# Kernel tuning notes

Measured on AMD Instinct MI355X. Metric: run time of the kernel, lower is better.

## Reference

```python
import jax, jax.numpy as jnp
import numpy as np

B, NSTEPS = 256, 128
I, H, V = 128, 1024, 1024  # input_size, hidden_size, output_size
SOS = 0


def setup_inputs() -> dict:
    key = jax.random.key(0)
    ks = jax.random.split(key, 9)
    s = 0.02
    return {
        "z": jax.random.normal(ks[0], (B, I), dtype=jnp.float32),
        "inputs": jax.random.randint(ks[1], (NSTEPS, B), 0, V, dtype=jnp.int64),
        "temperature": 10,  # randn() < 10 always -> teacher forcing every step
        "embed_w": jax.random.normal(ks[2], (V, H), dtype=jnp.float32) * s,
        "z2h_w": jax.random.normal(ks[3], (H, I), dtype=jnp.float32) * s,
        "z2h_b": jnp.zeros((H,), dtype=jnp.float32),
        "gru_w_ih": jax.random.normal(ks[4], (3 * H, H + I), dtype=jnp.float32) * s,
        "gru_b_ih": jnp.zeros((3 * H,), dtype=jnp.float32),
        "gru_w_hh": jax.random.normal(ks[5], (3 * H, H), dtype=jnp.float32) * s,
        "gru_b_hh": jnp.zeros((3 * H,), dtype=jnp.float32),
        "out_w": jax.random.normal(ks[6], (V, H + I), dtype=jnp.float32) * s,
        "out_b": jnp.zeros((V,), dtype=jnp.float32),
    }


def _gru_cell(x, h, w_ih, b_ih, w_hh, b_hh):
    # PyTorch GRU cell math
    gi = x @ w_ih.T + b_ih          # [B, 3H]
    gh = h @ w_hh.T + b_hh          # [B, 3H]
    i_r, i_z, i_n = jnp.split(gi, 3, axis=1)
    h_r, h_z, h_n = jnp.split(gh, 3, axis=1)
    r = jax.nn.sigmoid(i_r + h_r)
    zg = jax.nn.sigmoid(i_z + h_z)
    n = jnp.tanh(i_n + r * h_n)
    return (1.0 - zg) * n + zg * h


def reference(z, inputs, temperature, embed_w, z2h_w, z2h_b,
              gru_w_ih, gru_b_ih, gru_w_hh, gru_b_hh, out_w, out_b):
    # hidden init: z2h(z), n_layers=1 -> single [B, H] state
    h0 = z @ z2h_w.T + z2h_b
    tok0 = jnp.full((z.shape[0],), SOS, dtype=inputs.dtype)

    def step(carry, tok_next):
        tok, h = carry
        emb = jax.nn.relu(embed_w[tok])            # [B, H]
        x = jnp.concatenate([emb, z], axis=1)      # [B, H+I]
        h = _gru_cell(x, h, gru_w_ih, gru_b_ih, gru_w_hh, gru_b_hh)
        o = jnp.concatenate([h, z], axis=1) @ out_w.T + out_b  # [B, V]
        # teacher forcing (temperature >> randn always true): next input = inputs[i]
        return (tok_next, h), o

    (_, _), outs = jax.lax.scan(step, (tok0, h0), inputs)  # outs: [NSTEPS, B, V]
    return outs.transpose(1, 0, 2)  # [B, NSTEPS, V]
```

## Files before the change

### kernel.cpp

```cpp
#include <hip/hip_runtime.h>
#include <stdint.h>


#define NSTEP 128

typedef unsigned short u16;
typedef unsigned int u32;
typedef __attribute__((ext_vector_type(8))) short bf16x8;
typedef __attribute__((ext_vector_type(4))) int i32x4;
typedef __attribute__((ext_vector_type(4))) float f32x4;

typedef __attribute__((address_space(3))) void lds_void;
typedef const __attribute__((address_space(1))) void glb_void;
#define GLD16(g, l) __builtin_amdgcn_global_load_lds((glb_void*)(g), (lds_void*)(l), 16, 0, 0)
#define GLD16C(g, l) __builtin_amdgcn_global_load_lds((glb_void*)(g), (lds_void*)(l), 16, 0, 17)
#define CFENCE() asm volatile("" ::: "memory")
#define SCHEDB() __builtin_amdgcn_sched_barrier(0)

#if __has_builtin(__builtin_amdgcn_exp2f)
#define EXP2(x) __builtin_amdgcn_exp2f(x)
#else
#define EXP2(x) exp2f(x)
#endif
#if __has_builtin(__builtin_amdgcn_rcpf)
#define RCP(x) __builtin_amdgcn_rcpf(x)
#else
#define RCP(x) (1.0f / (x))
#endif

__device__ __forceinline__ u16 f2bf(float f) {
    u32 u = __float_as_uint(f);
    u = (u + 0x7FFFu + ((u >> 16) & 1u)) >> 16;
    return (u16)u;
}
__device__ __forceinline__ float fsigmoid(float x) {
    return RCP(1.f + EXP2(x * -1.44269504f));
}
__device__ __forceinline__ float ftanh(float x) {
    x = fminf(fmaxf(x, -18.f), 18.f);
    float t = EXP2(x * 2.88539008f);
    return (t - 1.f) * RCP(t + 1.f);
}

__device__ __forceinline__ void gloadf(float& d, const float* a) {
    asm volatile("global_load_dword %0, %1, off" : "=&v"(d) : "v"(a) : "memory");
}
__device__ __forceinline__ void gloadi4(i32x4& d, const int* a) {
    asm volatile("global_load_dwordx4 %0, %1, off" : "=&v"(d) : "v"(a) : "memory");
}
__device__ __forceinline__ void gstore_short_c(u16* a, u32 v) {
    asm volatile("global_store_short %0, %1, off sc0 sc1" ::"v"(a), "v"(v) : "memory");
}
__device__ __forceinline__ void gstoref(float* a, float v) {
    asm volatile("global_store_dword %0, %1, off" ::"v"(a), "v"(v) : "memory");
}

__global__ void cast_k(const float* __restrict__ src, int ld, int off, int relu,
                       u16* __restrict__ dst, int n) {
    for (int i = blockIdx.x * blockDim.x + threadIdx.x; i < n; i += gridDim.x * blockDim.x) {
        int row = i >> 10, col = i & 1023;
        float v = src[(long)row * ld + off + col];
        if (relu) v = fmaxf(v, 0.f);
        dst[i] = f2bf(v);
    }
}

__global__ void smallgemm_k(const float* __restrict__ z, const float* __restrict__ W,
                            int ldw, int off, const float* __restrict__ bias,
                            const float* __restrict__ bias2, int n2max,
                            float* __restrict__ C, u16* __restrict__ Cbf, int N) {
    int n = blockIdx.x;
    int b = threadIdx.x;
    float acc = bias[n] + ((bias2 && n < n2max) ? bias2[n] : 0.f);
    const float* zr = z + b * 128;
    const float* wr = W + (long)n * ldw + off;
#pragma unroll 8
    for (int k = 0; k < 128; ++k) acc += zr[k] * wr[k];
    C[b * N + n] = acc;
    if (Cbf) Cbf[b * N + n] = f2bf(acc);
}

__global__ __launch_bounds__(256) void egemm_k(const u16* __restrict__ A,
                                               const u16* __restrict__ W,
                                               float* __restrict__ C) {
    __shared__ __align__(16) u16 lds[2][160 * 64];
    int tid = threadIdx.x, lane = tid & 63, wv = tid >> 6;
    int r0 = (blockIdx.x & 31) * 32;
    int n0 = (blockIdx.x >> 5) * 128;

    f32x4 acc[2][2];
#pragma unroll
    for (int m = 0; m < 2; ++m)
#pragma unroll
        for (int n = 0; n < 2; ++n) acc[m][n] = (f32x4){0.f, 0.f, 0.f, 0.f};

    auto stage = [&](int k0, int bufi) {
#pragma unroll
        for (int r = 0; r < 5; ++r) {
            int L = r * 256 + tid;
            int row = L >> 3;
            int c4 = (L & 7) ^ (row & 7);
            const u16* src = (row < 32)
                                 ? A + (long)(r0 + row) * 1024 + k0 + c4 * 8
                                 : W + (long)(n0 + row - 32) * 1024 + k0 + c4 * 8;
            GLD16(src, &lds[bufi][L * 8]);
        }
    };
    stage(0, 0);
    stage(64, 1);
    for (int it = 0; it < 16; ++it) {
        if (it < 15) asm volatile("s_waitcnt vmcnt(5)" ::: "memory");
        else         asm volatile("s_waitcnt vmcnt(0)" ::: "memory");
        __builtin_amdgcn_s_barrier();
        const char* base = (const char*)&lds[it & 1][0];
        bf16x8 af[2][2], bfr[2][2];
#pragma unroll
        for (int ks = 0; ks < 2; ++ks)
#pragma unroll
            for (int q = 0; q < 2; ++q) {
                int kb = ks * 64 + ((lane >> 4) << 4);
                int rowa = q * 16 + (lane & 15);
                af[ks][q] = *(const bf16x8*)(base + rowa * 128 + (kb ^ ((rowa & 7) << 4)));
                int rowb = 32 + wv * 32 + q * 16 + (lane & 15);
                bfr[ks][q] = *(const bf16x8*)(base + rowb * 128 + (kb ^ ((rowb & 7) << 4)));
            }
#pragma unroll
        for (int ks = 0; ks < 2; ++ks)
#pragma unroll
            for (int m = 0; m < 2; ++m)
#pragma unroll
                for (int n = 0; n < 2; ++n)
                    acc[m][n] = __builtin_amdgcn_mfma_f32_16x16x32_bf16(af[ks][m], bfr[ks][n],
                                                                        acc[m][n], 0, 0, 0);
        asm volatile("s_waitcnt lgkmcnt(0)" ::: "memory");
        __builtin_amdgcn_s_barrier();
        if (it + 2 < 16) stage((it + 2) * 64, it & 1);
    }
#pragma unroll
    for (int m = 0; m < 2; ++m)
#pragma unroll
        for (int n = 0; n < 2; ++n)
#pragma unroll
            for (int r = 0; r < 4; ++r) {
                int row = r0 + m * 16 + ((lane >> 4) << 2) + r;
                int col = n0 + wv * 32 + n * 16 + (lane & 15);
                C[(long)row * 3072 + col] = acc[m][n][r];
            }
}

__global__ __launch_bounds__(256, 1) void decoder_k(
    const u16* __restrict__ Whh,
    const u16* __restrict__ Wout,
    const float* __restrict__ E,
    const float* __restrict__ Zih2,
    const float* __restrict__ Zout,
    const float* __restrict__ bhh,
    const int* __restrict__ toks,
    const float* __restrict__ h0f,
    u16* __restrict__ Hx,
    float* __restrict__ out,
    u32* __restrict__ flags) {
    __shared__ __align__(16) char L[163840];
    const int tid = threadIdx.x, lane = tid & 63, wv = tid >> 6;
    const int bid = blockIdx.x;
    const int rB = bid >> 6;
    const int c = bid & 63;

#pragma unroll
    for (int r = 0; r < 8; ++r) {
        int l = r * 256 + tid, row = l >> 7, ck = (l & 127) ^ (row & 15);
        GLD16(Whh + (long)(c * 16 + row) * 1024 + ck * 8, &L[65536 + l * 16]);
    }
#pragma unroll
    for (int r = 0; r < 8; ++r) {
        int l = r * 256 + tid, row = l >> 7, ck = (l & 127) ^ (row & 15);
        GLD16(Whh + (long)(1024 + c * 16 + row) * 1024 + ck * 8, &L[98304 + l * 16]);
    }
    asm volatile("s_waitcnt vmcnt(0)" ::: "memory");
    __builtin_amdgcn_s_barrier();
    bf16x8 w0[32], w1[32];
#pragma unroll
    for (int it = 0; it < 8; ++it)
#pragma unroll
        for (int ks = 0; ks < 4; ++ks) {
            int row = lane & 15, kc = it * 16 + ks * 4 + (lane >> 4);
            w0[it * 4 + ks] = *(const bf16x8*)(L + 65536 + row * 2048 + ((kc ^ row) << 4));
            w1[it * 4 + ks] = *(const bf16x8*)(L + 98304 + row * 2048 + ((kc ^ row) << 4));
        }
    asm volatile("s_waitcnt lgkmcnt(0)" ::: "memory");
    __builtin_amdgcn_s_barrier();
#pragma unroll
    for (int r = 0; r < 8; ++r) {
        int l = r * 256 + tid, row = l >> 7, ck = (l & 127) ^ (row & 15);
        GLD16(Whh + (long)(2048 + c * 16 + row) * 1024 + ck * 8, &L[l * 16]);
    }
#pragma unroll
    for (int r = 0; r < 8; ++r) {
        int l = r * 256 + tid, row = l >> 7, ck = (l & 127) ^ (row & 15);
        GLD16(Wout + (long)(c * 16 + row) * 1024 + ck * 8, &L[32768 + l * 16]);
    }
    asm volatile("s_waitcnt vmcnt(0)" ::: "memory");
    __builtin_amdgcn_s_barrier();

    const int bbase = rB * 64 + wv * 16 + ((lane >> 4) << 2);
    const int j = c * 16 + (lane & 15);
    const float bhn = bhh[2048 + j];
    float hprev[4], zi0[4], zi1[4], zi2[4], zo[4];
#pragma unroll
    for (int r = 0; r < 4; ++r) {
        int b = bbase + r;
        hprev[r] = h0f[b * 1024 + j];
        zi0[r] = Zih2[(long)b * 3072 + j];
        zi1[r] = Zih2[(long)b * 3072 + 1024 + j];
        zi2[r] = Zih2[(long)b * 3072 + 2048 + j];
        zo[r] = Zout[b * 1024 + j];
    }

    float ec0[4], ec1[4], ec2[4], en0[4], en1[4], en2[4];
#pragma unroll
    for (int r = 0; r < 4; ++r) {
        const float* eb = E + j;
        gloadf(en0[r], eb);
        gloadf(en1[r], eb + 1024);
        gloadf(en2[r], eb + 2048);
    }

    for (int s = 0; s <= NSTEP; ++s) {
        i32x4 tokv;
        if (s < NSTEP) gloadi4(tokv, toks + s * 256 + bbase);

        const u16* hsrc = Hx + (size_t)(s & 1) * 262144;
        auto stage = [&](int ch) {
            char* dst = L + 65536 + (ch % 6) * 16384;
            int k0 = ch * 128;
#pragma unroll
            for (int r = 0; r < 4; ++r) {
                int l = r * 256 + tid, row = l >> 4, ck = (l & 15) ^ (row & 15);
                GLD16C(hsrc + (long)(rB * 64 + row) * 1024 + k0 + ck * 8, dst + l * 16);
            }
        };
        stage(0);
        stage(1);
        stage(2);
        stage(3);
        CFENCE();

        if (s >= 1) {
            if (tid < 64) {
                const u32 tgt = (u32)s;
                const u32* gf = flags + (rB << 6) + 32;
                while (true) {
                    u32 v = __hip_atomic_load(gf + (lane & 31), __ATOMIC_RELAXED,
                                              __HIP_MEMORY_SCOPE_AGENT);
                    if (__all(v >= tgt)) break;
                    __builtin_amdgcn_s_sleep(1);
                }
            }
            __builtin_amdgcn_s_barrier();
        }

        f32x4 a0 = {0.f, 0.f, 0.f, 0.f}, a1 = a0, a2 = a0, aO = a0;
#pragma unroll
        for (int it = 0; it < 8; ++it) {
            if (it < 4) stage(it + 4);
            if (it < 4)       asm volatile("s_waitcnt vmcnt(16)" ::: "memory");
            else if (it == 4) asm volatile("s_waitcnt vmcnt(12)" ::: "memory");
            else if (it == 5) asm volatile("s_waitcnt vmcnt(8)" ::: "memory");
            else if (it == 6) asm volatile("s_waitcnt vmcnt(4)" ::: "memory");
            else              asm volatile("s_waitcnt vmcnt(0)" ::: "memory");
            SCHEDB();
            __builtin_amdgcn_s_barrier();
            const char* Ab = L + 65536 + (it % 6) * 16384;
            bf16x8 af[4];
#pragma unroll
            for (int ks = 0; ks < 4; ++ks) {
                int row = wv * 16 + (lane & 15), kc = ks * 4 + (lane >> 4);
                af[ks] = *(const bf16x8*)(Ab + row * 256 + ((kc ^ (row & 15)) << 4));
            }
#pragma unroll
            for (int ks = 0; ks < 4; ++ks)
                a0 = __builtin_amdgcn_mfma_f32_16x16x32_bf16(af[ks], w0[it * 4 + ks], a0, 0, 0, 0);
#pragma unroll
            for (int ks = 0; ks < 4; ++ks)
                a1 = __builtin_amdgcn_mfma_f32_16x16x32_bf16(af[ks], w1[it * 4 + ks], a1, 0, 0, 0);
#pragma unroll
            for (int ks = 0; ks < 4; ++ks) {
                int row = lane & 15, kc = it * 16 + ks * 4 + (lane >> 4);
                bf16x8 wg = *(const bf16x8*)(L + row * 2048 + ((kc ^ row) << 4));
                a2 = __builtin_amdgcn_mfma_f32_16x16x32_bf16(af[ks], wg, a2, 0, 0, 0);
            }
#pragma unroll
            for (int ks = 0; ks < 4; ++ks) {
                int row = lane & 15, kc = it * 16 + ks * 4 + (lane >> 4);
                bf16x8 wo = *(const bf16x8*)(L + 32768 + row * 2048 + ((kc ^ row) << 4));
                aO = __builtin_amdgcn_mfma_f32_16x16x32_bf16(af[ks], wo, aO, 0, 0, 0);
            }
        }
        if (s < NSTEP) {
#pragma unroll
            for (int r = 0; r < 4; ++r) {
                ec0[r] = en0[r];
                ec1[r] = en1[r];
                ec2[r] = en2[r];
            }
        }

        if (s < NSTEP) {
            u16* hdst = Hx + (size_t)((s + 1) & 1) * 262144;
#pragma unroll
            for (int r = 0; r < 4; ++r) {
                float rg = fsigmoid(ec0[r] + zi0[r] + a0[r]);
                float zg = fsigmoid(ec1[r] + zi1[r] + a1[r]);
                float nn = ftanh(ec2[r] + zi2[r] + rg * (a2[r] + bhn));
                float hv = (1.f - zg) * nn + zg * hprev[r];
                hprev[r] = hv;
                gstore_short_c(hdst + (bbase + r) * 1024 + j, (u32)f2bf(hv));
            }
        }
        if (s >= 1) {
#pragma unroll
            for (int r = 0; r < 4; ++r)
                gstoref(out + (long)(bbase + r) * 131072 + (long)(s - 1) * 1024 + j,
                        aO[r] + zo[r]);
        }
        if (s < NSTEP) {
#pragma unroll
            for (int r = 0; r < 4; ++r) {
                const float* eb = E + (long)tokv[r] * 3072 + j;
                gloadf(en0[r], eb);
                gloadf(en1[r], eb + 1024);
                gloadf(en2[r], eb + 2048);
            }
            if (s >= 1) asm volatile("s_waitcnt vmcnt(16)" ::: "memory");
            else        asm volatile("s_waitcnt vmcnt(12)" ::: "memory");
            SCHEDB();
            __builtin_amdgcn_s_barrier();
            if (tid == 0)
                __hip_atomic_store(&flags[bid], (u32)(s + 1), __ATOMIC_RELAXED,
                                   __HIP_MEMORY_SCOPE_AGENT);
            if (tid < 64) {
                const u32 tgt = (u32)(s + 1);
                const u32* gf = flags + (rB << 6);
                while (true) {
                    u32 v = __hip_atomic_load(gf + (lane & 31), __ATOMIC_RELAXED,
                                              __HIP_MEMORY_SCOPE_AGENT);
                    if (__all(v >= tgt)) break;
                    __builtin_amdgcn_s_sleep(1);
                }
            }
            __builtin_amdgcn_s_barrier();
        }
    }
}

extern "C" void kernel_launch(void* const* d_in, const int* in_sizes, int n_in,
                              void* d_out, int out_size, void* d_ws, size_t ws_size,
                              hipStream_t stream) {
    const float* z = (const float*)d_in[0];
    const int* toks = (const int*)d_in[1];
    const float* embed_w = (const float*)d_in[3];
    const float* z2h_w = (const float*)d_in[4];
    const float* z2h_b = (const float*)d_in[5];
    const float* w_ih = (const float*)d_in[6];
    const float* b_ih = (const float*)d_in[7];
    const float* w_hh = (const float*)d_in[8];
    const float* b_hh = (const float*)d_in[9];
    const float* out_w = (const float*)d_in[10];
    const float* out_b = (const float*)d_in[11];
    float* out = (float*)d_out;

    char* ws = (char*)d_ws;
    size_t off = 0;
    auto alloc = [&](size_t bytes) {
        char* p = ws + off;
        off += (bytes + 255) & ~(size_t)255;
        return p;
    };
    u16* Whh_bf = (u16*)alloc(3072ull * 1024 * 2);
    u16* Wout_bf = (u16*)alloc(1024ull * 1024 * 2);
    u16* Wihh_bf = (u16*)alloc(3072ull * 1024 * 2);
    u16* Emb_bf = (u16*)alloc(1024ull * 1024 * 2);
    float* E = (float*)alloc(1024ull * 3072 * 4);
    float* Zih = (float*)alloc(256ull * 3072 * 4);
    float* Zout = (float*)alloc(256ull * 1024 * 4);
    float* hf = (float*)alloc(256ull * 1024 * 4);
    u16* Hx = (u16*)alloc(2ull * 256 * 1024 * 2);
    u32* flags = (u32*)alloc(1024);

    hipMemsetAsync(flags, 0, 1024, stream);
    cast_k<<<2048, 256, 0, stream>>>(w_hh, 1024, 0, 0, Whh_bf, 3072 * 1024);
    cast_k<<<2048, 256, 0, stream>>>(out_w, 1152, 0, 0, Wout_bf, 1024 * 1024);
    cast_k<<<2048, 256, 0, stream>>>(w_ih, 1152, 0, 0, Wihh_bf, 3072 * 1024);
    cast_k<<<1024, 256, 0, stream>>>(embed_w, 1024, 0, 1, Emb_bf, 1024 * 1024);
    smallgemm_k<<<1024, 256, 0, stream>>>(z, z2h_w, 128, 0, z2h_b, nullptr, 0, hf, Hx, 1024);
    smallgemm_k<<<3072, 256, 0, stream>>>(z, w_ih, 1152, 1024, b_ih, b_hh, 2048, Zih, nullptr, 3072);
    smallgemm_k<<<1024, 256, 0, stream>>>(z, out_w, 1152, 1024, out_b, nullptr, 0, Zout, nullptr, 1024);
    egemm_k<<<768, 256, 0, stream>>>(Emb_bf, Wihh_bf, E);

    decoder_k<<<256, 256, 0, stream>>>(Whh_bf, Wout_bf, E, Zih, Zout, b_hh, toks, hf, Hx, out,
                                       flags);
}
```

Baseline: 1.117 ms.

## Split decoder into 512 XCC-local blocks with register-resident output weights

```diff
diff --git a/kernel.cpp b/kernel.cpp
--- a/kernel.cpp
+++ b/kernel.cpp
@@ -14,6 +14,7 @@
 typedef const __attribute__((address_space(1))) void glb_void;
 #define GLD16(g, l) __builtin_amdgcn_global_load_lds((glb_void*)(g), (lds_void*)(l), 16, 0, 0)
 #define GLD16C(g, l) __builtin_amdgcn_global_load_lds((glb_void*)(g), (lds_void*)(l), 16, 0, 17)
+#define GLD16S0(g, l) __builtin_amdgcn_global_load_lds((glb_void*)(g), (lds_void*)(l), 16, 0, 1)
 #define CFENCE() asm volatile("" ::: "memory")
 #define SCHEDB() __builtin_amdgcn_sched_barrier(0)
 
@@ -51,8 +52,29 @@
 __device__ __forceinline__ void gstore_short_c(u16* a, u32 v) {
     asm volatile("global_store_short %0, %1, off sc0 sc1" ::"v"(a), "v"(v) : "memory");
 }
+__device__ __forceinline__ void gstore_short_p(u16* a, u32 v) {
+    asm volatile("global_store_short %0, %1, off" ::"v"(a), "v"(v) : "memory");
+}
 __device__ __forceinline__ void gstoref(float* a, float v) {
     asm volatile("global_store_dword %0, %1, off" ::"v"(a), "v"(v) : "memory");
+}
+__device__ __forceinline__ void gstoreu32_c(u32* a, u32 v) {
+    asm volatile("global_store_dword %0, %1, off sc0 sc1" ::"v"(a), "v"(v) : "memory");
+}
+__device__ __forceinline__ void gstoreu32_p(u32* a, u32 v) {
+    asm volatile("global_store_dword %0, %1, off" ::"v"(a), "v"(v) : "memory");
+}
+__device__ __forceinline__ u32 pollload_s0(const u32* a) {
+    u32 d;
+    asm volatile("global_load_dword %0, %1, off sc0\n\ts_waitcnt vmcnt(0)"
+                 : "=&v"(d) : "v"(a) : "memory");
+    return d;
+}
+__device__ __forceinline__ u32 pollload_c(const u32* a) {
+    u32 d;
+    asm volatile("global_load_dword %0, %1, off sc0 sc1\n\ts_waitcnt vmcnt(0)"
+                 : "=&v"(d) : "v"(a) : "memory");
+    return d;
 }
 
 __global__ void cast_k(const float* __restrict__ src, int ld, int off, int relu,
@@ -148,7 +170,7 @@
             }
 }
 
-__global__ __launch_bounds__(256, 1) void decoder_k(
+__global__ __launch_bounds__(128, 1) void decoder_k(
     const u16* __restrict__ Whh,
     const u16* __restrict__ Wout,
     const float* __restrict__ E,
@@ -159,50 +181,68 @@
     const float* __restrict__ h0f,
     u16* __restrict__ Hx,
     float* __restrict__ out,
-    u32* __restrict__ flags) {
-    __shared__ __align__(16) char L[163840];
+    u32* __restrict__ flags,
+    u32* __restrict__ xcctab) {
+    __shared__ __align__(16) char L[81920];
     const int tid = threadIdx.x, lane = tid & 63, wv = tid >> 6;
     const int bid = blockIdx.x;
-    const int rB = bid >> 6;
-    const int c = bid & 63;
-
-#pragma unroll
-    for (int r = 0; r < 8; ++r) {
-        int l = r * 256 + tid, row = l >> 7, ck = (l & 127) ^ (row & 15);
-        GLD16(Whh + (long)(c * 16 + row) * 1024 + ck * 8, &L[65536 + l * 16]);
-    }
-#pragma unroll
-    for (int r = 0; r < 8; ++r) {
-        int l = r * 256 + tid, row = l >> 7, ck = (l & 127) ^ (row & 15);
-        GLD16(Whh + (long)(1024 + c * 16 + row) * 1024 + ck * 8, &L[98304 + l * 16]);
-    }
+    const int g = bid & 7;
+    const int c = bid >> 3;
+
+    u32 myxcc;
+    asm volatile("s_getreg_b32 %0, hwreg(HW_REG_XCC_ID)" : "=s"(myxcc));
+    if (tid == 0) gstoreu32_c(xcctab + bid, myxcc);
     asm volatile("s_waitcnt vmcnt(0)" ::: "memory");
     __builtin_amdgcn_s_barrier();
-    bf16x8 w0[32], w1[32];
-#pragma unroll
-    for (int it = 0; it < 8; ++it)
-#pragma unroll
-        for (int ks = 0; ks < 4; ++ks) {
-            int row = lane & 15, kc = it * 16 + ks * 4 + (lane >> 4);
-            w0[it * 4 + ks] = *(const bf16x8*)(L + 65536 + row * 2048 + ((kc ^ row) << 4));
-            w1[it * 4 + ks] = *(const bf16x8*)(L + 98304 + row * 2048 + ((kc ^ row) << 4));
-        }
-    asm volatile("s_waitcnt lgkmcnt(0)" ::: "memory");
+    int lok;
+    if (tid < 64) {
+        u32 xv;
+        while (true) {
+            xv = pollload_c(xcctab + (g << 6) + lane);
+            SCHEDB();
+            if (__all(xv != 0xFFFFFFFFu)) break;
+            __builtin_amdgcn_s_sleep(1);
+        }
+        u32 x0 = __builtin_amdgcn_readfirstlane(xv);
+        int ok = __all(xv == x0) ? 1 : 0;
+        if (tid == 0) *(volatile int*)&L[0] = ok;
+    }
     __builtin_amdgcn_s_barrier();
-#pragma unroll
-    for (int r = 0; r < 8; ++r) {
-        int l = r * 256 + tid, row = l >> 7, ck = (l & 127) ^ (row & 15);
+    lok = *(volatile int*)&L[0];
+    __builtin_amdgcn_s_barrier();
+
+    bf16x8 w0[32], w1[32], wO[32];
+    auto wload = [&](const u16* base, int rowoff, bf16x8* wreg) {
+#pragma unroll
+        for (int r = 0; r < 16; ++r) {
+            int l = r * 128 + tid, row = l >> 7, ck = (l & 127) ^ (row & 15);
+            GLD16(base + (long)(rowoff + c * 16 + row) * 1024 + ck * 8, &L[32768 + l * 16]);
+        }
+        asm volatile("s_waitcnt vmcnt(0)" ::: "memory");
+        __builtin_amdgcn_s_barrier();
+#pragma unroll
+        for (int it = 0; it < 8; ++it)
+#pragma unroll
+            for (int ks = 0; ks < 4; ++ks) {
+                int row = lane & 15, kc = it * 16 + ks * 4 + (lane >> 4);
+                wreg[it * 4 + ks] =
+                    *(const bf16x8*)(L + 32768 + row * 2048 + ((kc ^ row) << 4));
+            }
+        asm volatile("s_waitcnt lgkmcnt(0)" ::: "memory");
+        __builtin_amdgcn_s_barrier();
+    };
+    wload(Whh, 0, w0);
+    wload(Whh, 1024, w1);
+    wload(Wout, 0, wO);
+#pragma unroll
+    for (int r = 0; r < 16; ++r) {
+        int l = r * 128 + tid, row = l >> 7, ck = (l & 127) ^ (row & 15);
         GLD16(Whh + (long)(2048 + c * 16 + row) * 1024 + ck * 8, &L[l * 16]);
-    }
-#pragma unroll
-    for (int r = 0; r < 8; ++r) {
-        int l = r * 256 + tid, row = l >> 7, ck = (l & 127) ^ (row & 15);
-        GLD16(Wout + (long)(c * 16 + row) * 1024 + ck * 8, &L[32768 + l * 16]);
     }
     asm volatile("s_waitcnt vmcnt(0)" ::: "memory");
     __builtin_amdgcn_s_barrier();
 
-    const int bbase = rB * 64 + wv * 16 + ((lane >> 4) << 2);
+    const int bbase = g * 32 + wv * 16 + ((lane >> 4) << 2);
     const int j = c * 16 + (lane & 15);
     const float bhn = bhh[2048 + j];
     float hprev[4], zi0[4], zi1[4], zi2[4], zo[4];
@@ -231,12 +271,17 @@
 
         const u16* hsrc = Hx + (size_t)(s & 1) * 262144;
         auto stage = [&](int ch) {
-            char* dst = L + 65536 + (ch % 6) * 16384;
+            char* dst = L + 32768 + (ch % 6) * 8192;
             int k0 = ch * 128;
 #pragma unroll
             for (int r = 0; r < 4; ++r) {
-                int l = r * 256 + tid, row = l >> 4, ck = (l & 15) ^ (row & 15);
-                GLD16C(hsrc + (long)(rB * 64 + row) * 1024 + k0 + ck * 8, dst + l * 16);
+                int i = wv * 4 + r;
+                int row = i * 4 + (lane >> 4);
+                int ck = (lane & 15) ^ (row & 15);
+                const u16* sp = hsrc + (long)(g * 32 + row) * 1024 + k0 + ck * 8;
+                char* d = dst + i * 1024 + lane * 16;
+                if (lok) GLD16S0(sp, d);
+                else     GLD16C(sp, d);
             }
         };
         stage(0);
@@ -248,10 +293,11 @@
         if (s >= 1) {
             if (tid < 64) {
                 const u32 tgt = (u32)s;
-                const u32* gf = flags + (rB << 6) + 32;
+                const u32* gf = flags + (g << 6) + 32;
                 while (true) {
-                    u32 v = __hip_atomic_load(gf + (lane & 31), __ATOMIC_RELAXED,
-                                              __HIP_MEMORY_SCOPE_AGENT);
+                    u32 v = lok ? pollload_s0(gf + (lane & 31))
+                                : __hip_atomic_load(gf + (lane & 31), __ATOMIC_RELAXED,
+                                                    __HIP_MEMORY_SCOPE_AGENT);
                     if (__all(v >= tgt)) break;
                     __builtin_amdgcn_s_sleep(1);
                 }
@@ -270,7 +316,7 @@
             else              asm volatile("s_waitcnt vmcnt(0)" ::: "memory");
             SCHEDB();
             __builtin_amdgcn_s_barrier();
-            const char* Ab = L + 65536 + (it % 6) * 16384;
+            const char* Ab = L + 32768 + (it % 6) * 8192;
             bf16x8 af[4];
 #pragma unroll
             for (int ks = 0; ks < 4; ++ks) {
@@ -290,11 +336,8 @@
                 a2 = __builtin_amdgcn_mfma_f32_16x16x32_bf16(af[ks], wg, a2, 0, 0, 0);
             }
 #pragma unroll
-            for (int ks = 0; ks < 4; ++ks) {
-                int row = lane & 15, kc = it * 16 + ks * 4 + (lane >> 4);
-                bf16x8 wo = *(const bf16x8*)(L + 32768 + row * 2048 + ((kc ^ row) << 4));
-                aO = __builtin_amdgcn_mfma_f32_16x16x32_bf16(af[ks], wo, aO, 0, 0, 0);
-            }
+            for (int ks = 0; ks < 4; ++ks)
+                aO = __builtin_amdgcn_mfma_f32_16x16x32_bf16(af[ks], wO[it * 4 + ks], aO, 0, 0, 0);
         }
         if (s < NSTEP) {
 #pragma unroll
@@ -314,7 +357,10 @@
                 float nn = ftanh(ec2[r] + zi2[r] + rg * (a2[r] + bhn));
                 float hv = (1.f - zg) * nn + zg * hprev[r];
                 hprev[r] = hv;
-                gstore_short_c(hdst + (bbase + r) * 1024 + j, (u32)f2bf(hv));
+                u32 hb = (u32)f2bf(hv);
+                u16* hp = hdst + (bbase + r) * 1024 + j;
+                if (lok) gstore_short_p(hp, hb);
+                else     gstore_short_c(hp, hb);
             }
         }
         if (s >= 1) {
@@ -335,15 +381,20 @@
             else        asm volatile("s_waitcnt vmcnt(12)" ::: "memory");
             SCHEDB();
             __builtin_amdgcn_s_barrier();
-            if (tid == 0)
-                __hip_atomic_store(&flags[bid], (u32)(s + 1), __ATOMIC_RELAXED,
-                                   __HIP_MEMORY_SCOPE_AGENT);
+            if (tid == 0) {
+                u32* fp = flags + (g << 6) + c;
+                if (lok) gstoreu32_p(fp, (u32)(s + 1));
+                else
+                    __hip_atomic_store(fp, (u32)(s + 1), __ATOMIC_RELAXED,
+                                       __HIP_MEMORY_SCOPE_AGENT);
+            }
             if (tid < 64) {
                 const u32 tgt = (u32)(s + 1);
-                const u32* gf = flags + (rB << 6);
+                const u32* gf = flags + (g << 6);
                 while (true) {
-                    u32 v = __hip_atomic_load(gf + (lane & 31), __ATOMIC_RELAXED,
-                                              __HIP_MEMORY_SCOPE_AGENT);
+                    u32 v = lok ? pollload_s0(gf + (lane & 31))
+                                : __hip_atomic_load(gf + (lane & 31), __ATOMIC_RELAXED,
+                                                    __HIP_MEMORY_SCOPE_AGENT);
                     if (__all(v >= tgt)) break;
                     __builtin_amdgcn_s_sleep(1);
                 }
@@ -385,9 +436,11 @@
     float* Zout = (float*)alloc(256ull * 1024 * 4);
     float* hf = (float*)alloc(256ull * 1024 * 4);
     u16* Hx = (u16*)alloc(2ull * 256 * 1024 * 2);
-    u32* flags = (u32*)alloc(1024);
-
-    hipMemsetAsync(flags, 0, 1024, stream);
+    u32* flags = (u32*)alloc(2048);
+    u32* xcctab = (u32*)alloc(2048);
+
+    hipMemsetAsync(flags, 0, 2048, stream);
+    hipMemsetAsync(xcctab, 0xFF, 2048, stream);
     cast_k<<<2048, 256, 0, stream>>>(w_hh, 1024, 0, 0, Whh_bf, 3072 * 1024);
     cast_k<<<2048, 256, 0, stream>>>(out_w, 1152, 0, 0, Wout_bf, 1024 * 1024);
     cast_k<<<2048, 256, 0, stream>>>(w_ih, 1152, 0, 0, Wihh_bf, 3072 * 1024);
@@ -397,6 +450,6 @@
     smallgemm_k<<<1024, 256, 0, stream>>>(z, out_w, 1152, 1024, out_b, nullptr, 0, Zout, nullptr, 1024);
     egemm_k<<<768, 256, 0, stream>>>(Emb_bf, Wihh_bf, E);
 
-    decoder_k<<<256, 256, 0, stream>>>(Whh_bf, Wout_bf, E, Zih, Zout, b_hh, toks, hf, Hx, out,
-                                       flags);
-}
+    decoder_k<<<512, 128, 0, stream>>>(Whh_bf, Wout_bf, E, Zih, Zout, b_hh, toks, hf, Hx, out,
+                                       flags, xcctab);
+}
```

After: 1.740 ms. +55.8%, slower.
